# Kernel tuning notes

Hardware: AMD Instinct MI355X
Metric: run time of the kernel (lower is better)

Reference implementation:

```python
import jax, jax.numpy as jnp
import numpy as np

NODE_TYPES = ["patient", "visit", "symptom", "procedure", "disease", "drug"]
N = {"patient": 20000, "visit": 100000, "symptom": 4000, "procedure": 8000,
     "disease": 10000, "drug": 4000}
D = 128          # embedding_dim == hidden_channels
N_LAYERS = 4     # conv1..conv4
# (src, dst) per relation; reverse edges included so every node type gets messages
REL = [("patient", "visit"), ("visit", "patient"),
       ("visit", "symptom"), ("symptom", "visit"),
       ("visit", "procedure"), ("procedure", "visit"),
       ("visit", "disease"), ("disease", "visit"),
       ("visit", "drug"), ("drug", "visit")]
E_FWD = {("patient", "visit"): 100000, ("visit", "symptom"): 300000,
         ("visit", "procedure"): 200000, ("visit", "disease"): 250000,
         ("visit", "drug"): 300000}
EI_NAMES = ["ei_pv", "ei_vp", "ei_vs", "ei_sv", "ei_vpr", "ei_prv",
            "ei_vd", "ei_dv", "ei_vdr", "ei_drv"]
E_LABEL = 200000


def setup_inputs() -> dict:
    key = jax.random.key(0)
    ks = iter(jax.random.split(key, 64))
    inp = {}
    for nt in NODE_TYPES:
        inp[f"node_id_{nt}"] = jnp.arange(N[nt], dtype=jnp.int32)
        inp[f"emb_{nt}"] = jax.random.normal(next(ks), (N[nt], D), jnp.float32)
    for name, (src, dst) in zip(EI_NAMES, REL):
        e = E_FWD.get((src, dst), E_FWD.get((dst, src)))
        row = jax.random.randint(next(ks), (e,), 0, N[src], dtype=jnp.int32)
        col = jax.random.randint(next(ks), (e,), 0, N[dst], dtype=jnp.int32)
        inp[name] = jnp.stack([row, col])
    R = len(REL)
    inp["W_l"] = jax.random.normal(next(ks), (N_LAYERS, R, D, D), jnp.float32) * 0.05
    inp["b_l"] = jnp.zeros((N_LAYERS, R, D), jnp.float32)
    inp["W_r"] = jax.random.normal(next(ks), (N_LAYERS, R, D, D), jnp.float32) * 0.05
    inp["cls_w1"] = jax.random.normal(next(ks), (2 * D, D), jnp.float32) * 0.05
    inp["cls_b1"] = jnp.zeros((D,), jnp.float32)
    inp["cls_w2"] = jax.random.normal(next(ks), (D, 1), jnp.float32) * 0.05
    inp["cls_b2"] = jnp.zeros((1,), jnp.float32)
    row = jax.random.randint(next(ks), (E_LABEL,), 0, N["visit"], dtype=jnp.int32)
    col = jax.random.randint(next(ks), (E_LABEL,), 0, N["drug"], dtype=jnp.int32)
    inp["edge_label_index"] = jnp.stack([row, col])
    inp["edge_label"] = jax.random.bernoulli(next(ks), 0.5, (E_LABEL,)).astype(jnp.float32)
    return inp


def _hetero_sage_layer(x, eis, Wl, bl, Wr):
    # to_hetero semantics: out[dst] = sum over edge types (src,rel,dst) of
    #   SAGEConv_rel: lin_l(mean_j x[src][j]) + lin_r(x[dst])   (PyG defaults)
    out = {nt: jnp.zeros_like(v) for nt, v in x.items()}
    for r, (src, dst) in enumerate(REL):
        ei = eis[r]
        n_dst = x[dst].shape[0]
        msg = jax.ops.segment_sum(x[src][ei[0]], ei[1], num_segments=n_dst)
        deg = jax.ops.segment_sum(jnp.ones((ei.shape[1],), x[src].dtype), ei[1],
                                  num_segments=n_dst)
        mean = msg / jnp.maximum(deg, 1.0)[:, None]  # empty segments stay 0 as in PyG
        out[dst] = out[dst] + mean @ Wl[r] + bl[r] + x[dst] @ Wr[r]
    return out


def reference(node_id_patient, node_id_visit, node_id_symptom, node_id_procedure,
              node_id_disease, node_id_drug,
              emb_patient, emb_visit, emb_symptom, emb_procedure, emb_disease, emb_drug,
              ei_pv, ei_vp, ei_vs, ei_sv, ei_vpr, ei_prv, ei_vd, ei_dv, ei_vdr, ei_drv,
              W_l, b_l, W_r, cls_w1, cls_b1, cls_w2, cls_b2,
              edge_label_index, edge_label):
    x = {"patient": emb_patient[node_id_patient],
         "visit": emb_visit[node_id_visit],
         "symptom": emb_symptom[node_id_symptom],
         "procedure": emb_procedure[node_id_procedure],
         "disease": emb_disease[node_id_disease],
         "drug": emb_drug[node_id_drug]}
    eis = [ei_pv, ei_vp, ei_vs, ei_sv, ei_vpr, ei_prv, ei_vd, ei_dv, ei_vdr, ei_drv]
    for l in range(N_LAYERS):
        x = _hetero_sage_layer(x, eis, W_l[l], b_l[l], W_r[l])
        if l < N_LAYERS - 1:  # relu after conv1..conv3 only; dropout is eval-mode identity
            x = {k: jax.nn.relu(v) for k, v in x.items()}
    # Classifier: gather visit/drug node features per labeled edge, concat, MLP
    zv = x["visit"][edge_label_index[0]]
    zd = x["drug"][edge_label_index[1]]
    h = jax.nn.relu(jnp.concatenate([zv, zd], axis=-1) @ cls_w1 + cls_b1)
    pred = (h @ cls_w2 + cls_b2).reshape(-1)
    # BCE with logits: softplus(z) - z*y, mean-reduced
    loss = jnp.mean(jax.nn.softplus(pred) - pred * edge_label)
    return loss, pred
```

## Files before the change

kernel.cpp:

```cpp
#include <hip/hip_runtime.h>
#include <cmath>


typedef _Float16 f16x8 __attribute__((ext_vector_type(8)));
typedef float f32x4 __attribute__((ext_vector_type(4)));

#define NREL 10
#define NCOUNTS 546000
#define NEDGES  2300000
#define NVISIT  100000
#define NVEDGES 1150000
#define PLW 546816
#define WT_ELEMS (4 * PLW + 69632)
#define XELEMS 18688000UL
#define SELEMS 5888000UL
#define NBKT 873
#define BCAP 5056

struct BkMeta {
  const int* ei[NREL]; int E[NREL]; int cbc[NREL]; int ndst[NREL];
  int sh[NREL]; int bb[NREL]; int nb[NREL];
};
struct PreMeta {
  const float* emb[6]; const int* nid[6]; int rows[6]; int off[6];
  const float* W_l; const float* b_l; const float* W_r; const float* cw1;
  _Float16* Wt; float* visitSumB;
};
struct MTask {
  const _Float16* AH0; const _Float16* AL0;
  const _Float16* AH1; const _Float16* AL1;
  const _Float16* W;
  const float* bias;
  _Float16* outH; _Float16* outL;
  int M, blkOff, K, relu;
};
struct MMeta { MTask t[6]; int nTasks; };
struct F1Meta {
  const int* rp[5]; _Float16* mH[5]; _Float16* mL[5]; int aM[5]; int aOff[5];
  int nAgg; int aggTotal;
  const _Float16* gAH[5]; const _Float16* gAL[5]; const _Float16* gW[5];
  _Float16* gY[5]; int gM[5]; int gOff[5]; int nG;
};

__global__ __launch_bounds__(256) void pre_all(PreMeta pm, BkMeta bm,
                                               _Float16* __restrict__ H,
                                               _Float16* __restrict__ L,
                                               int* __restrict__ bcur,
                                               int* __restrict__ bdata) {
  __shared__ int cnt[128];
  __shared__ int base[128];
  __shared__ unsigned short rnk[4096];
  int b = blockIdx.x;
  int tid = threadIdx.x;
  if (b < 37500) {
    int t = b / 6250;
    int i = (b % 6250) * 256 + tid;
    if (i >= pm.rows[t] * 16) return;
    int row = i >> 4, q = i & 15;
    int s = pm.nid[t][row];
    const float* p = pm.emb[t] + (size_t)s * 128 + q * 8;
    float4 v0 = *(const float4*)p;
    float4 v1 = *(const float4*)(p + 4);
    float v[8] = {v0.x, v0.y, v0.z, v0.w, v1.x, v1.y, v1.z, v1.w};
    f16x8 h, l;
    #pragma unroll
    for (int j = 0; j < 8; ++j) {
      h[j] = (_Float16)v[j];
      l[j] = (_Float16)(v[j] - (float)h[j]);
    }
    size_t o = (size_t)(pm.off[t] + row) * 128 + q * 8;
    *(f16x8*)(H + o) = h;
    *(f16x8*)(L + o) = l;
    return;
  }
  if (b < 41726) {
    const int visitRel[5] = {0, 3, 5, 7, 9};
    const int inRel[5] = {1, 2, 4, 6, 8};
    int gid = (b - 37500) * 256 + tid;
    if (gid < 1048576) {
      int l = gid >> 18, o = gid & 262143;
      float val; size_t wbase; int n, k, Kpad;
      if (o < 163840) {
        int t = o >> 15, e = o & 32767;
        k = e >> 7; n = e & 127; Kpad = 264;
        int r = inRel[t];
        val = (k < 128) ? pm.W_l[(size_t)(l * 10 + r) * 16384 + k * 128 + n]
                        : pm.W_r[(size_t)(l * 10 + r) * 16384 + (k - 128) * 128 + n];
        wbase = (size_t)l * PLW + t * 67584;
      } else if (o < 245760) {
        int q = (o - 163840) >> 14, e = (o - 163840) & 16383;
        k = e >> 7; n = e & 127; Kpad = 136;
        val = pm.W_l[(size_t)(l * 10 + visitRel[q]) * 16384 + k * 128 + n];
        wbase = (size_t)l * PLW + 337920 + q * 34816;
      } else {
        int e = o - 245760;
        k = e >> 7; n = e & 127; Kpad = 136;
        val = 0.f;
        #pragma unroll
        for (int q = 0; q < 5; ++q)
          val += pm.W_r[(size_t)(l * 10 + visitRel[q]) * 16384 + k * 128 + n];
        wbase = (size_t)l * PLW + 512000;
      }
      _Float16 h = (_Float16)val;
      _Float16 lo = (_Float16)(val - (float)h);
      pm.Wt[wbase + (size_t)n * Kpad + k] = h;
      pm.Wt[wbase + (size_t)(128 + n) * Kpad + k] = lo;
    } else if (gid < 1081344) {
      int e = gid - 1048576;
      int k = e >> 7, n = e & 127;
      float val = pm.cw1[(size_t)k * 128 + n];
      _Float16 h = (_Float16)val;
      _Float16 lo = (_Float16)(val - (float)h);
      size_t wbase = (size_t)4 * PLW + (k < 128 ? 0 : 34816);
      int kk = k & 127;
      pm.Wt[wbase + (size_t)n * 136 + kk] = h;
      pm.Wt[wbase + (size_t)(128 + n) * 136 + kk] = lo;
    } else if (gid < 1081856) {
      int e = gid - 1081344;
      int l = e >> 7, c = e & 127;
      float val = 0.f;
      #pragma unroll
      for (int q = 0; q < 5; ++q) val += pm.b_l[(l * 10 + visitRel[q]) * 128 + c];
      pm.visitSumB[e] = val;
    }
    return;
  }
  int fb = b - 41726;
  int r = fb / 74;
  int bx = fb - r * 74;
  int E = bm.E[r], sh = bm.sh[r], bb = bm.bb[r], nb = bm.nb[r];
  if (tid < 128) cnt[tid] = 0;
  __syncthreads();
  int e0 = bx * 4096;
  if (e0 >= E) return;
  const int* dstp = bm.ei[r] + E;
  const int* srcp = bm.ei[r];
  #pragma unroll
  for (int i = 0; i < 16; ++i) {
    int e = e0 + i * 256 + tid;
    if (e < E) {
      int bk = dstp[e] >> sh;
      rnk[i * 256 + tid] = (unsigned short)atomicAdd(&cnt[bk], 1);
    }
  }
  __syncthreads();
  if (tid < nb && cnt[tid] > 0) base[tid] = atomicAdd(&bcur[bb + tid], cnt[tid]);
  __syncthreads();
  #pragma unroll
  for (int i = 0; i < 16; ++i) {
    int e = e0 + i * 256 + tid;
    if (e < E) {
      int d = dstp[e];
      int bk = d >> sh;
      int pos = base[bk] + (int)rnk[i * 256 + tid];
      if (pos < BCAP)
        bdata[(size_t)(bb + bk) * BCAP + pos] = ((d & ((1 << sh) - 1)) << 17) | srcp[e];
    }
  }
}

__global__ __launch_bounds__(256) void bkt_p2a(BkMeta bm, const int* __restrict__ bcur,
                                               const int* __restrict__ bdata,
                                               int* __restrict__ counts) {
  __shared__ int hist[2048];
  int g = blockIdx.x;
  int r = 0;
  #pragma unroll
  for (int i = 1; i < NREL; ++i) if (g >= bm.bb[i]) r = i;
  int lb = g - bm.bb[r];
  int sh = bm.sh[r], dpb = 1 << sh;
  int tid = threadIdx.x;
  for (int d = tid; d < dpb; d += 256) hist[d] = 0;
  __syncthreads();
  int cnt = bcur[g]; if (cnt > BCAP) cnt = BCAP;
  const int* bd = bdata + (size_t)g * BCAP;
  for (int i = tid; i < cnt; i += 256) atomicAdd(&hist[((unsigned)bd[i]) >> 17], 1);
  __syncthreads();
  int dBase = lb << sh;
  int dMax = bm.ndst[r] - dBase; if (dMax > dpb) dMax = dpb;
  for (int d = tid; d < dMax; d += 256) counts[bm.cbc[r] + dBase + d] = hist[d];
}

__global__ __launch_bounds__(1024) void scan1(const int* __restrict__ counts,
                                              int* __restrict__ partials) {
  __shared__ int s[1024];
  int i = blockIdx.x * 1024 + threadIdx.x;
  s[threadIdx.x] = (i < NCOUNTS) ? counts[i] : 0;
  __syncthreads();
  for (int off = 512; off > 0; off >>= 1) {
    if (threadIdx.x < off) s[threadIdx.x] += s[threadIdx.x + off];
    __syncthreads();
  }
  if (threadIdx.x == 0) partials[blockIdx.x] = s[0];
}

__global__ __launch_bounds__(1024) void scan2(int* __restrict__ partials, int nb) {
  __shared__ int s[1024];
  int t = threadIdx.x;
  int v = (t < nb) ? partials[t] : 0;
  s[t] = v;
  __syncthreads();
  for (int off = 1; off < 1024; off <<= 1) {
    int add = (t >= off) ? s[t - off] : 0;
    __syncthreads();
    s[t] += add;
    __syncthreads();
  }
  if (t < nb) partials[t] = s[t] - v;
}

__global__ __launch_bounds__(1024) void scan3(const int* __restrict__ counts,
                                              int* __restrict__ prefix,
                                              const int* __restrict__ partials) {
  __shared__ int s[1024];
  int t = threadIdx.x;
  int i = blockIdx.x * 1024 + t;
  int v = (i < NCOUNTS) ? counts[i] : 0;
  s[t] = v;
  __syncthreads();
  for (int off = 1; off < 1024; off <<= 1) {
    int add = (t >= off) ? s[t - off] : 0;
    __syncthreads();
    s[t] += add;
    __syncthreads();
  }
  int P = partials[blockIdx.x] + s[t] - v;
  if (i < NCOUNTS) prefix[i] = P;
  if (blockIdx.x == 0 && t == 0) prefix[NCOUNTS] = NEDGES;
}

__global__ __launch_bounds__(256) void bkt_p2b(BkMeta bm, const int* __restrict__ bcur,
                                               const int* __restrict__ bdata,
                                               const int* __restrict__ prefix,
                                               int* __restrict__ esrc) {
  __shared__ int pk[BCAP];
  __shared__ int srt[BCAP];
  __shared__ int cur[2048];
  __shared__ int part[256];
  __shared__ int baseSh;
  int g = blockIdx.x;
  int r = 0;
  #pragma unroll
  for (int i = 1; i < NREL; ++i) if (g >= bm.bb[i]) r = i;
  int lb = g - bm.bb[r];
  int sh = bm.sh[r], dpb = 1 << sh;
  int tid = threadIdx.x;
  int cnt = bcur[g]; if (cnt > BCAP) cnt = BCAP;
  const int* bd = bdata + (size_t)g * BCAP;
  for (int d = tid; d < dpb; d += 256) cur[d] = 0;
  for (int i = tid; i < cnt; i += 256) pk[i] = bd[i];
  __syncthreads();
  for (int i = tid; i < cnt; i += 256) atomicAdd(&cur[((unsigned)pk[i]) >> 17], 1);
  __syncthreads();
  int seg = (dpb + 255) >> 8;
  int s = 0;
  int b0 = tid * seg;
  for (int j = 0; j < seg; ++j) {
    int idx = b0 + j;
    if (idx < dpb) { int v = cur[idx]; cur[idx] = s; s += v; }
  }
  part[tid] = s;
  __syncthreads();
  for (int off = 1; off < 256; off <<= 1) {
    int add = (tid >= off) ? part[tid - off] : 0;
    __syncthreads();
    part[tid] += add;
    __syncthreads();
  }
  int myoff = part[tid] - s;
  for (int j = 0; j < seg; ++j) {
    int idx = b0 + j;
    if (idx < dpb) cur[idx] += myoff;
  }
  if (tid == 0) baseSh = prefix[bm.cbc[r] + (lb << sh)];
  __syncthreads();
  for (int i = tid; i < cnt; i += 256) {
    int p = pk[i];
    int pos = atomicAdd(&cur[((unsigned)p) >> 17], 1);
    srt[pos] = p & 0x1FFFF;
  }
  __syncthreads();
  int base = baseSh;
  for (int i = tid; i < cnt; i += 256) esrc[base + i] = srt[i];
}

__global__ __launch_bounds__(256) void merge_visit(const int* __restrict__ prefix,
                                                   const int* __restrict__ esrc,
                                                   int* __restrict__ mprefix,
                                                   int2* __restrict__ mesrc) {
  const int cbc[5]  = {0, 124000, 232000, 342000, 446000};
  const int yoff[5] = {0, 20000, 24000, 32000, 42000};
  int v = blockIdx.x * 256 + threadIdx.x;
  if (v >= NVISIT) return;
  int e0[5], e1[5];
  int base = 0;
  #pragma unroll
  for (int q = 0; q < 5; ++q) {
    e0[q] = prefix[cbc[q] + v];
    e1[q] = prefix[cbc[q] + v + 1];
    base += e0[q] - prefix[cbc[q]];
  }
  mprefix[v] = base;
  if (v == NVISIT - 1) {
    int t = base;
    #pragma unroll
    for (int q = 0; q < 5; ++q) t += e1[q] - e0[q];
    mprefix[NVISIT] = t;
  }
  int pos = base;
  #pragma unroll
  for (int q = 0; q < 5; ++q) {
    int d = e1[q] - e0[q];
    if (d > 0) {
      int wb = __float_as_int(1.f / (float)d);
      for (int e = e0[q]; e < e1[q]; ++e)
        mesrc[pos++] = make_int2(yoff[q] + esrc[e], wb);
    }
  }
}

__global__ __launch_bounds__(256, 8) void fused1(F1Meta f,
                                                 const _Float16* __restrict__ xvH,
                                                 const int* __restrict__ esrc) {
  int b = blockIdx.x;
  int tid = threadIdx.x;
  if (b < f.aggTotal) {
    int t = 0;
    #pragma unroll
    for (int i = 1; i < 5; ++i) if (i < f.nAgg && b >= f.aOff[i]) t = i;
    int row = (b - f.aOff[t]) * 16 + (tid >> 4);
    if (row >= f.aM[t]) return;
    int q = tid & 15;
    const int* rp = f.rp[t];
    int e0 = rp[row], e1 = rp[row + 1];
    float a[8];
    #pragma unroll
    for (int j = 0; j < 8; ++j) a[j] = 0.f;
    int e = e0;
    for (; e + 4 <= e1; e += 4) {
      int s0 = esrc[e], s1 = esrc[e + 1], s2 = esrc[e + 2], s3 = esrc[e + 3];
      f16x8 v0 = *(const f16x8*)(xvH + (size_t)s0 * 128 + q * 8);
      f16x8 v1 = *(const f16x8*)(xvH + (size_t)s1 * 128 + q * 8);
      f16x8 v2 = *(const f16x8*)(xvH + (size_t)s2 * 128 + q * 8);
      f16x8 v3 = *(const f16x8*)(xvH + (size_t)s3 * 128 + q * 8);
      #pragma unroll
      for (int j = 0; j < 8; ++j)
        a[j] += ((float)v0[j] + (float)v1[j]) + ((float)v2[j] + (float)v3[j]);
    }
    for (; e < e1; ++e) {
      int s = esrc[e];
      f16x8 v = *(const f16x8*)(xvH + (size_t)s * 128 + q * 8);
      #pragma unroll
      for (int j = 0; j < 8; ++j) a[j] += (float)v[j];
    }
    float inv = (e1 > e0) ? 1.f / (float)(e1 - e0) : 0.f;
    f16x8 h, l;
    #pragma unroll
    for (int j = 0; j < 8; ++j) {
      float v = a[j] * inv;
      h[j] = (_Float16)v;
      l[j] = (_Float16)(v - (float)h[j]);
    }
    size_t o = (size_t)row * 128 + q * 8;
    *(f16x8*)(f.mH[t] + o) = h;
    *(f16x8*)(f.mL[t] + o) = l;
    return;
  }
  b -= f.aggTotal;
  int g = 0;
  #pragma unroll
  for (int i = 1; i < 5; ++i) if (i < f.nG && b >= f.gOff[i]) g = i;
  int blockRow = (b - f.gOff[g]) * 32;
  int lane = tid & 63, wave = tid >> 6;
  int quad = lane >> 4, lm = lane & 15;
  int wr = wave >> 1, wc = wave & 1;
  const _Float16* AH = f.gAH[g];
  const _Float16* AL = f.gAL[g];
  const _Float16* W = f.gW[g];
  int M = f.gM[g];
  int ar = blockRow + wr * 16 + lm;
  if (ar >= M) ar = M - 1;
  f32x4 acc[4];
  #pragma unroll
  for (int nt = 0; nt < 4; ++nt) acc[nt] = (f32x4){0.f, 0.f, 0.f, 0.f};
  for (int ks = 0; ks < 128; ks += 32) {
    f16x8 ah = *(const f16x8*)(AH + (size_t)ar * 128 + ks + quad * 8);
    f16x8 al = *(const f16x8*)(AL + (size_t)ar * 128 + ks + quad * 8);
    #pragma unroll
    for (int nt = 0; nt < 4; ++nt) {
      int n = wc * 64 + nt * 16 + lm;
      f16x8 bh = *(const f16x8*)(W + (size_t)n * 136 + ks + quad * 8);
      f16x8 bl = *(const f16x8*)(W + (size_t)(128 + n) * 136 + ks + quad * 8);
      acc[nt] = __builtin_amdgcn_mfma_f32_16x16x32_f16(ah, bh, acc[nt], 0, 0, 0);
      acc[nt] = __builtin_amdgcn_mfma_f32_16x16x32_f16(ah, bl, acc[nt], 0, 0, 0);
      acc[nt] = __builtin_amdgcn_mfma_f32_16x16x32_f16(al, bh, acc[nt], 0, 0, 0);
    }
  }
  _Float16* Y = f.gY[g];
  #pragma unroll
  for (int i = 0; i < 4; ++i) {
    int grow = blockRow + wr * 16 + quad * 4 + i;
    if (grow >= M) continue;
    #pragma unroll
    for (int nt = 0; nt < 4; ++nt)
      Y[(size_t)grow * 128 + wc * 64 + nt * 16 + lm] = (_Float16)acc[nt][i];
  }
}

__global__ __launch_bounds__(256) void agg_visit(const int* __restrict__ mprefix,
                                                 const int2* __restrict__ mesrc,
                                                 const _Float16* __restrict__ YH,
                                                 _Float16* __restrict__ xvH,
                                                 _Float16* __restrict__ xvL, int doRelu) {
  int row = blockIdx.x * 16 + (threadIdx.x >> 4);
  if (row >= NVISIT) return;
  int q = threadIdx.x & 15;
  size_t o = (size_t)row * 128 + q * 8;
  f16x8 h0 = *(f16x8*)(xvH + o);
  f16x8 l0 = *(f16x8*)(xvL + o);
  float a[8];
  #pragma unroll
  for (int j = 0; j < 8; ++j) a[j] = (float)h0[j] + (float)l0[j];
  int e0 = mprefix[row], e1 = mprefix[row + 1];
  int e = e0;
  for (; e + 4 <= e1; e += 4) {
    int2 p0 = mesrc[e], p1 = mesrc[e + 1], p2 = mesrc[e + 2], p3 = mesrc[e + 3];
    f16x8 v0 = *(const f16x8*)(YH + (size_t)p0.x * 128 + q * 8);
    f16x8 v1 = *(const f16x8*)(YH + (size_t)p1.x * 128 + q * 8);
    f16x8 v2 = *(const f16x8*)(YH + (size_t)p2.x * 128 + q * 8);
    f16x8 v3 = *(const f16x8*)(YH + (size_t)p3.x * 128 + q * 8);
    float w0 = __int_as_float(p0.y), w1 = __int_as_float(p1.y);
    float w2 = __int_as_float(p2.y), w3 = __int_as_float(p3.y);
    #pragma unroll
    for (int j = 0; j < 8; ++j)
      a[j] += (w0 * (float)v0[j] + w1 * (float)v1[j]) +
              (w2 * (float)v2[j] + w3 * (float)v3[j]);
  }
  for (; e < e1; ++e) {
    int2 p = mesrc[e];
    f16x8 v = *(const f16x8*)(YH + (size_t)p.x * 128 + q * 8);
    float w = __int_as_float(p.y);
    #pragma unroll
    for (int j = 0; j < 8; ++j) a[j] += w * (float)v[j];
  }
  f16x8 h, l;
  #pragma unroll
  for (int j = 0; j < 8; ++j) {
    float v = doRelu ? fmaxf(a[j], 0.f) : a[j];
    h[j] = (_Float16)v;
    l[j] = (_Float16)(v - (float)h[j]);
  }
  *(f16x8*)(xvH + o) = h;
  *(f16x8*)(xvL + o) = l;
}

__global__ __launch_bounds__(256, 2) void mgemm(MMeta mm) {
  int b = blockIdx.x;
  int ti = 0;
  for (int i = 1; i < mm.nTasks; ++i) if (b >= mm.t[i].blkOff) ti = i;
  MTask tk = mm.t[ti];
  int blockRow = (b - tk.blkOff) * 128;
  int Kpad = tk.K + 8;

  __shared__ _Float16 Ash[2][128][72];
  int tid = threadIdx.x;
  int wave = tid >> 6, lane = tid & 63;
  int quad = lane >> 4, lm = lane & 15;
  int wr = wave >> 1, wc = wave & 1;

  f32x4 acc[4][4];
  #pragma unroll
  for (int i = 0; i < 4; ++i)
    #pragma unroll
    for (int j = 0; j < 4; ++j) acc[i][j] = (f32x4){0.f, 0.f, 0.f, 0.f};

  const _Float16* wrowH[4];
  const _Float16* wrowL[4];
  #pragma unroll
  for (int nt = 0; nt < 4; ++nt) {
    int n = wc * 64 + nt * 16 + lm;
    wrowH[nt] = tk.W + (size_t)n * Kpad;
    wrowL[nt] = tk.W + (size_t)(128 + n) * Kpad;
  }

  int sr = tid >> 1, sk = (tid & 1) * 32;
  int gr = blockRow + sr; if (gr >= tk.M) gr = tk.M - 1;
  for (int k0 = 0; k0 < tk.K; k0 += 64) {
    const _Float16* AH = (k0 < 128) ? tk.AH0 : tk.AH1;
    const _Float16* AL = (k0 < 128) ? tk.AL0 : tk.AL1;
    size_t abase = (size_t)gr * 128 + (k0 & 127) + sk;
    #pragma unroll
    for (int c = 0; c < 4; ++c) {
      *(f16x8*)&Ash[0][sr][sk + c * 8] = *(const f16x8*)(AH + abase + c * 8);
      *(f16x8*)&Ash[1][sr][sk + c * 8] = *(const f16x8*)(AL + abase + c * 8);
    }
    __syncthreads();
    #pragma unroll
    for (int ks = 0; ks < 64; ks += 32) {
      int kf = k0 + ks + quad * 8;
      f16x8 bh[4], bl[4];
      #pragma unroll
      for (int nt = 0; nt < 4; ++nt) {
        bh[nt] = *(const f16x8*)(wrowH[nt] + kf);
        bl[nt] = *(const f16x8*)(wrowL[nt] + kf);
      }
      #pragma unroll
      for (int mt = 0; mt < 4; ++mt) {
        int r = wr * 64 + mt * 16 + lm;
        f16x8 ah = *(const f16x8*)&Ash[0][r][ks + quad * 8];
        f16x8 al = *(const f16x8*)&Ash[1][r][ks + quad * 8];
        #pragma unroll
        for (int nt = 0; nt < 4; ++nt) {
          acc[mt][nt] = __builtin_amdgcn_mfma_f32_16x16x32_f16(ah, bh[nt], acc[mt][nt], 0, 0, 0);
          acc[mt][nt] = __builtin_amdgcn_mfma_f32_16x16x32_f16(ah, bl[nt], acc[mt][nt], 0, 0, 0);
          acc[mt][nt] = __builtin_amdgcn_mfma_f32_16x16x32_f16(al, bh[nt], acc[mt][nt], 0, 0, 0);
        }
      }
    }
    __syncthreads();
  }

  float bv[4];
  #pragma unroll
  for (int nt = 0; nt < 4; ++nt)
    bv[nt] = tk.bias ? tk.bias[wc * 64 + nt * 16 + lm] : 0.f;
  #pragma unroll
  for (int mt = 0; mt < 4; ++mt) {
    #pragma unroll
    for (int i = 0; i < 4; ++i) {
      int grow = blockRow + wr * 64 + mt * 16 + quad * 4 + i;
      if (grow >= tk.M) continue;
      size_t ob = (size_t)grow * 128 + wc * 64 + lm;
      #pragma unroll
      for (int nt = 0; nt < 4; ++nt) {
        float v = acc[mt][nt][i] + bv[nt];
        if (tk.relu) v = fmaxf(v, 0.f);
        _Float16 h = (_Float16)v;
        tk.outH[ob + nt * 16] = h;
        if (tk.outL) tk.outL[ob + nt * 16] = (_Float16)(v - (float)h);
      }
    }
  }
}

__global__ __launch_bounds__(256) void cls_edge(
    const _Float16* __restrict__ UH, const _Float16* __restrict__ UL,
    const _Float16* __restrict__ VH, const _Float16* __restrict__ VL,
    const int* __restrict__ eli, const float* __restrict__ w2,
    const float* __restrict__ b2, const float* __restrict__ y,
    float* __restrict__ lossOut, float* __restrict__ pred, int M) {
  __shared__ float lsum[4];
  int tid = threadIdx.x;
  int q = tid & 15;
  int lane = tid & 63;
  float w2v[8];
  #pragma unroll
  for (int j = 0; j < 8; ++j) w2v[j] = w2[q * 8 + j];
  float bias = b2[0];
  float lacc = 0.f;
  int e0 = blockIdx.x * 128 + (tid >> 4);
  #pragma unroll
  for (int p = 0; p < 8; ++p) {
    int e = e0 + p * 16;
    if (e < M) {
      int vi = eli[e], di = eli[M + e];
      size_t uo = (size_t)vi * 128 + q * 8;
      size_t vo = (size_t)di * 128 + q * 8;
      f16x8 uh = *(const f16x8*)(UH + uo);
      f16x8 ul = *(const f16x8*)(UL + uo);
      f16x8 vh = *(const f16x8*)(VH + vo);
      f16x8 vl = *(const f16x8*)(VL + vo);
      float part = 0.f;
      #pragma unroll
      for (int j = 0; j < 8; ++j) {
        float t = ((float)uh[j] + (float)ul[j]) + ((float)vh[j] + (float)vl[j]);
        part += fmaxf(t, 0.f) * w2v[j];
      }
      part += __shfl_xor(part, 1);
      part += __shfl_xor(part, 2);
      part += __shfl_xor(part, 4);
      part += __shfl_xor(part, 8);
      if (q == 0) {
        float z = part + bias;
        pred[e] = z;
        lacc += fmaxf(z, 0.f) + log1pf(expf(-fabsf(z))) - z * y[e];
      }
    }
  }
  lacc += __shfl_xor(lacc, 16);
  lacc += __shfl_xor(lacc, 32);
  if (lane == 0) lsum[tid >> 6] = lacc;
  __syncthreads();
  if (tid == 0)
    atomicAdd(lossOut, (lsum[0] + lsum[1] + lsum[2] + lsum[3]) * (1.0f / 200000.0f));
}

extern "C" void kernel_launch(void* const* d_in, const int* in_sizes, int n_in,
                              void* d_out, int out_size, void* d_ws, size_t ws_size,
                              hipStream_t stream) {
  static const int kRows[6] = {20000, 100000, 4000, 8000, 10000, 4000};
  static const int kOff[6]  = {0, 20000, 120000, 124000, 132000, 142000};
  static const int kSmallT[5]   = {0, 2, 3, 4, 5};
  static const int kInRel[5]    = {1, 2, 4, 6, 8};
  static const int kCbcIn[5]    = {100000, 120000, 224000, 332000, 442000};
  static const int kYOff[5]     = {0, 20000, 24000, 32000, 42000};
  static const int kBOff[5]     = {0, 157, 189, 252, 331};
  static const int kAggOff[5]   = {0, 1250, 1500, 2000, 2625};
  static const int kLeanOff[5]  = {0, 625, 750, 1000, 1313};
  const int kAggTotal = 2875, kLeanTotal = 1438;
  static const int kCbcA[NREL]  = {0, 100000, 120000, 124000, 224000,
                                   232000, 332000, 342000, 442000, 446000};
  static const int kEhA[NREL]   = {100000, 100000, 300000, 300000, 200000,
                                   200000, 250000, 250000, 300000, 300000};
  static const int kNdst[NREL]  = {100000, 20000, 4000, 100000, 8000,
                                   100000, 10000, 100000, 4000, 100000};
  static const int kSh[NREL]    = {11, 9, 5, 10, 7, 10, 7, 10, 5, 10};
  static const int kNB[NREL]    = {49, 40, 125, 98, 63, 98, 79, 98, 125, 98};
  static const int kBB[NREL]    = {0, 49, 89, 214, 312, 375, 473, 552, 650, 775};

  const float* W_l = (const float*)d_in[22];
  const float* b_l = (const float*)d_in[23];
  const float* W_r = (const float*)d_in[24];
  const float* cw1 = (const float*)d_in[25];
  const float* cb1 = (const float*)d_in[26];
  const float* cw2 = (const float*)d_in[27];
  const float* cb2 = (const float*)d_in[28];
  const int* eli = (const int*)d_in[29];
  const float* ylab = (const float*)d_in[30];

  _Float16* H = (_Float16*)d_ws;
  _Float16* L = H + XELEMS;
  _Float16* meanH = L + XELEMS;
  _Float16* meanL = meanH + SELEMS;
  _Float16* YH = meanL + SELEMS;
  _Float16* Wt = YH + SELEMS;
  int* prefix = (int*)(Wt + WT_ELEMS);
  int* counts = prefix + 546004;
  int* esrc = counts + NCOUNTS;
  int* partials = esrc + NEDGES;
  float* visitSumB = (float*)(partials + 1024);
  int* bcur = (int*)(visitSumB + 512);
  int* bdata = bcur + 1024;

  int* mprefix = counts;
  int2* mesrc = (int2*)bdata;

  _Float16* UH = meanH;
  _Float16* VH = meanH + (size_t)NVISIT * 128;
  _Float16* VL = VH + (size_t)4000 * 128;
  _Float16* UL = (_Float16*)prefix;

  BkMeta bm;
  for (int r = 0; r < NREL; ++r) {
    bm.ei[r] = (const int*)d_in[12 + r];
    bm.E[r] = kEhA[r];
    bm.cbc[r] = kCbcA[r];
    bm.ndst[r] = kNdst[r];
    bm.sh[r] = kSh[r];
    bm.bb[r] = kBB[r];
    bm.nb[r] = kNB[r];
  }

  hipMemsetAsync(bcur, 0, NBKT * sizeof(int), stream);
  hipMemsetAsync(d_out, 0, sizeof(float), stream);

  PreMeta pm;
  for (int t = 0; t < 6; ++t) {
    pm.nid[t] = (const int*)d_in[2 * t];
    pm.emb[t] = (const float*)d_in[2 * t + 1];
    pm.rows[t] = kRows[t];
    pm.off[t] = kOff[t];
  }
  pm.W_l = W_l; pm.b_l = b_l; pm.W_r = W_r; pm.cw1 = cw1;
  pm.Wt = Wt; pm.visitSumB = visitSumB;
  pre_all<<<dim3(42466), 256, 0, stream>>>(pm, bm, H, L, bcur, bdata);

  bkt_p2a<<<dim3(NBKT), 256, 0, stream>>>(bm, bcur, bdata, counts);
  scan1<<<534, 1024, 0, stream>>>(counts, partials);
  scan2<<<1, 1024, 0, stream>>>(partials, 534);
  scan3<<<534, 1024, 0, stream>>>(counts, prefix, partials);
  bkt_p2b<<<dim3(NBKT), 256, 0, stream>>>(bm, bcur, bdata, prefix, esrc);
  merge_visit<<<dim3((NVISIT + 255) / 256), 256, 0, stream>>>(prefix, esrc, mprefix, mesrc);

  _Float16* xvH = H + (size_t)kOff[1] * 128;
  _Float16* xvL = L + (size_t)kOff[1] * 128;

  for (int l = 0; l < 4; ++l) {
    int doRelu = (l < 3);
    int last = (l == 3);
    _Float16* LW = Wt + (size_t)l * PLW;

    F1Meta f1;
    if (!last) {
      for (int t = 0; t < 5; ++t) {
        f1.rp[t] = prefix + kCbcIn[t];
        f1.mH[t] = meanH + (size_t)kYOff[t] * 128;
        f1.mL[t] = meanL + (size_t)kYOff[t] * 128;
        f1.aM[t] = kRows[kSmallT[t]];
        f1.aOff[t] = kAggOff[t];
      }
      f1.nAgg = 5;
      f1.aggTotal = kAggTotal;
    } else {
      f1.rp[0] = prefix + kCbcIn[4];
      f1.mH[0] = meanH + (size_t)kYOff[4] * 128;
      f1.mL[0] = meanL + (size_t)kYOff[4] * 128;
      f1.aM[0] = 4000;
      f1.aOff[0] = 0;
      for (int t = 1; t < 5; ++t) { f1.rp[t] = nullptr; f1.mH[t] = nullptr; f1.mL[t] = nullptr; f1.aM[t] = 0; f1.aOff[t] = 0; }
      f1.nAgg = 1;
      f1.aggTotal = 250;
    }
    for (int q = 0; q < 5; ++q) {
      size_t so = (size_t)kOff[kSmallT[q]] * 128;
      f1.gAH[q] = H + so;
      f1.gAL[q] = L + so;
      f1.gW[q] = LW + 337920 + (size_t)q * 34816;
      f1.gY[q] = YH + (size_t)kYOff[q] * 128;
      f1.gM[q] = kRows[kSmallT[q]];
      f1.gOff[q] = kLeanOff[q];
    }
    f1.nG = 5;
    fused1<<<dim3(f1.aggTotal + kLeanTotal), 256, 0, stream>>>(f1, xvH, esrc);

    MMeta m;
    if (!last) {
      m.nTasks = 6;
      for (int t = 0; t < 5; ++t) {
        size_t mo = (size_t)kYOff[t] * 128;
        size_t so = (size_t)kOff[kSmallT[t]] * 128;
        m.t[t].AH0 = meanH + mo; m.t[t].AL0 = meanL + mo;
        m.t[t].AH1 = H + so;     m.t[t].AL1 = L + so;
        m.t[t].W = LW + (size_t)t * 67584;
        m.t[t].bias = b_l + (size_t)(l * 10 + kInRel[t]) * 128;
        m.t[t].outH = H + so;    m.t[t].outL = L + so;
        m.t[t].M = kRows[kSmallT[t]];
        m.t[t].blkOff = kBOff[t];
        m.t[t].K = 256;
        m.t[t].relu = doRelu;
      }
      m.t[5].AH0 = xvH; m.t[5].AL0 = xvL;
      m.t[5].AH1 = nullptr; m.t[5].AL1 = nullptr;
      m.t[5].W = LW + 512000;
      m.t[5].bias = visitSumB + l * 128;
      m.t[5].outH = xvH; m.t[5].outL = xvL;
      m.t[5].M = NVISIT;
      m.t[5].blkOff = 363;
      m.t[5].K = 128;
      m.t[5].relu = 0;
      mgemm<<<dim3(363 + 782), 256, 0, stream>>>(m);
    } else {
      size_t mo = (size_t)kYOff[4] * 128;
      size_t so = (size_t)kOff[5] * 128;
      m.nTasks = 2;
      m.t[0].AH0 = meanH + mo; m.t[0].AL0 = meanL + mo;
      m.t[0].AH1 = H + so;     m.t[0].AL1 = L + so;
      m.t[0].W = LW + (size_t)4 * 67584;
      m.t[0].bias = b_l + (size_t)(l * 10 + kInRel[4]) * 128;
      m.t[0].outH = H + so;    m.t[0].outL = L + so;
      m.t[0].M = 4000;
      m.t[0].blkOff = 0;
      m.t[0].K = 256;
      m.t[0].relu = 0;
      m.t[1].AH0 = xvH; m.t[1].AL0 = xvL;
      m.t[1].AH1 = nullptr; m.t[1].AL1 = nullptr;
      m.t[1].W = LW + 512000;
      m.t[1].bias = visitSumB + l * 128;
      m.t[1].outH = xvH; m.t[1].outL = xvL;
      m.t[1].M = NVISIT;
      m.t[1].blkOff = 32;
      m.t[1].K = 128;
      m.t[1].relu = 0;
      mgemm<<<dim3(32 + 782), 256, 0, stream>>>(m);
    }

    agg_visit<<<dim3(6250), 256, 0, stream>>>(mprefix, mesrc, YH, xvH, xvL, doRelu);
  }

  MMeta muv;
  muv.nTasks = 2;
  muv.t[0].AH0 = xvH; muv.t[0].AL0 = xvL;
  muv.t[0].AH1 = nullptr; muv.t[0].AL1 = nullptr;
  muv.t[0].W = Wt + (size_t)4 * PLW;
  muv.t[0].bias = cb1;
  muv.t[0].outH = UH; muv.t[0].outL = UL;
  muv.t[0].M = NVISIT;
  muv.t[0].blkOff = 0;
  muv.t[0].K = 128;
  muv.t[0].relu = 0;
  muv.t[1].AH0 = H + (size_t)kOff[5] * 128; muv.t[1].AL0 = L + (size_t)kOff[5] * 128;
  muv.t[1].AH1 = nullptr; muv.t[1].AL1 = nullptr;
  muv.t[1].W = Wt + (size_t)4 * PLW + 34816;
  muv.t[1].bias = nullptr;
  muv.t[1].outH = VH; muv.t[1].outL = VL;
  muv.t[1].M = 4000;
  muv.t[1].blkOff = 782;
  muv.t[1].K = 128;
  muv.t[1].relu = 0;
  mgemm<<<dim3(782 + 32), 256, 0, stream>>>(muv);

  const int ML = 200000;
  cls_edge<<<dim3((ML + 127) / 128), 256, 0, stream>>>(
      UH, UL, VH, VL, eli, cw2, cb2, ylab,
      (float*)d_out, (float*)d_out + 1, ML);
}
```

Measured before the change: 909.1 us.

## Spread embedding fp16 conversion across bucket-sort kernels to overlap work

The embedding gather and hi/lo fp16 split is taken out of the first preprocessing kernel and spread as extra blocks across the bucket count, bucket sort and visit merge kernels. Conversion blocks are also packed densely by global row offset, so the padded per-type block grid is gone. The aim is to fill the idle CUs left by the small, latency-bound sort kernels with this bandwidth-bound work, and to shorten the critical first kernel. In exchange, the later kernels carry more blocks, and the merge kernel's grid now depends on the conversion share assigned to it.

```diff
diff --git a/kernel.cpp b/kernel.cpp
--- a/kernel.cpp
+++ b/kernel.cpp
@@ -16,13 +16,15 @@
 #define SELEMS 5888000UL
 #define NBKT 873
 #define BCAP 5056
+#define NMERGE 391
+#define CONV_BLKS 9125
 
 struct BkMeta {
   const int* ei[NREL]; int E[NREL]; int cbc[NREL]; int ndst[NREL];
   int sh[NREL]; int bb[NREL]; int nb[NREL];
 };
 struct PreMeta {
-  const float* emb[6]; const int* nid[6]; int rows[6]; int off[6];
+  const float* emb[6]; const int* nid[6]; int off[6];
   const float* W_l; const float* b_l; const float* W_r; const float* cw1;
   _Float16* Wt; float* visitSumB;
 };
@@ -42,92 +44,97 @@
   _Float16* gY[5]; int gM[5]; int gOff[5]; int nG;
 };
 
-__global__ __launch_bounds__(256) void pre_all(PreMeta pm, BkMeta bm,
-                                               _Float16* __restrict__ H,
-                                               _Float16* __restrict__ L,
-                                               int* __restrict__ bcur,
-                                               int* __restrict__ bdata) {
+__device__ __forceinline__ void conv0_body(const PreMeta& pm, int bc, int tid,
+                                           _Float16* __restrict__ H,
+                                           _Float16* __restrict__ L) {
+  int i = bc * 256 + tid;
+  if (i >= 146000 * 16) return;
+  int g = i >> 4, q = i & 15;
+  int t = 0;
+  #pragma unroll
+  for (int k = 1; k < 6; ++k) if (g >= pm.off[k]) t = k;
+  int row = g - pm.off[t];
+  int s = pm.nid[t][row];
+  const float* p = pm.emb[t] + (size_t)s * 128 + q * 8;
+  float4 v0 = *(const float4*)p;
+  float4 v1 = *(const float4*)(p + 4);
+  float v[8] = {v0.x, v0.y, v0.z, v0.w, v1.x, v1.y, v1.z, v1.w};
+  f16x8 h, l;
+  #pragma unroll
+  for (int j = 0; j < 8; ++j) {
+    h[j] = (_Float16)v[j];
+    l[j] = (_Float16)(v[j] - (float)h[j]);
+  }
+  size_t o = (size_t)g * 128 + q * 8;
+  *(f16x8*)(H + o) = h;
+  *(f16x8*)(L + o) = l;
+}
+
+__device__ __forceinline__ void prep_body(const PreMeta& pm, int gid) {
+  const int visitRel[5] = {0, 3, 5, 7, 9};
+  const int inRel[5] = {1, 2, 4, 6, 8};
+  if (gid < 1048576) {
+    int l = gid >> 18, o = gid & 262143;
+    float val; size_t wbase; int n, k, Kpad;
+    if (o < 163840) {
+      int t = o >> 15, e = o & 32767;
+      k = e >> 7; n = e & 127; Kpad = 264;
+      int r = inRel[t];
+      val = (k < 128) ? pm.W_l[(size_t)(l * 10 + r) * 16384 + k * 128 + n]
+                      : pm.W_r[(size_t)(l * 10 + r) * 16384 + (k - 128) * 128 + n];
+      wbase = (size_t)l * PLW + t * 67584;
+    } else if (o < 245760) {
+      int q = (o - 163840) >> 14, e = (o - 163840) & 16383;
+      k = e >> 7; n = e & 127; Kpad = 136;
+      val = pm.W_l[(size_t)(l * 10 + visitRel[q]) * 16384 + k * 128 + n];
+      wbase = (size_t)l * PLW + 337920 + q * 34816;
+    } else {
+      int e = o - 245760;
+      k = e >> 7; n = e & 127; Kpad = 136;
+      val = 0.f;
+      #pragma unroll
+      for (int q = 0; q < 5; ++q)
+        val += pm.W_r[(size_t)(l * 10 + visitRel[q]) * 16384 + k * 128 + n];
+      wbase = (size_t)l * PLW + 512000;
+    }
+    _Float16 h = (_Float16)val;
+    _Float16 lo = (_Float16)(val - (float)h);
+    pm.Wt[wbase + (size_t)n * Kpad + k] = h;
+    pm.Wt[wbase + (size_t)(128 + n) * Kpad + k] = lo;
+  } else if (gid < 1081344) {
+    int e = gid - 1048576;
+    int k = e >> 7, n = e & 127;
+    float val = pm.cw1[(size_t)k * 128 + n];
+    _Float16 h = (_Float16)val;
+    _Float16 lo = (_Float16)(val - (float)h);
+    size_t wbase = (size_t)4 * PLW + (k < 128 ? 0 : 34816);
+    int kk = k & 127;
+    pm.Wt[wbase + (size_t)n * 136 + kk] = h;
+    pm.Wt[wbase + (size_t)(128 + n) * 136 + kk] = lo;
+  } else if (gid < 1081856) {
+    int e = gid - 1081344;
+    int l = e >> 7, c = e & 127;
+    float val = 0.f;
+    #pragma unroll
+    for (int q = 0; q < 5; ++q) val += pm.b_l[(l * 10 + visitRel[q]) * 128 + c];
+    pm.visitSumB[e] = val;
+  }
+}
+
+__global__ __launch_bounds__(256) void k1_p1_prep(BkMeta bm, PreMeta pm,
+                                                  int* __restrict__ bcur,
+                                                  int* __restrict__ bdata) {
   __shared__ int cnt[128];
   __shared__ int base[128];
   __shared__ unsigned short rnk[4096];
   int b = blockIdx.x;
   int tid = threadIdx.x;
-  if (b < 37500) {
-    int t = b / 6250;
-    int i = (b % 6250) * 256 + tid;
-    if (i >= pm.rows[t] * 16) return;
-    int row = i >> 4, q = i & 15;
-    int s = pm.nid[t][row];
-    const float* p = pm.emb[t] + (size_t)s * 128 + q * 8;
-    float4 v0 = *(const float4*)p;
-    float4 v1 = *(const float4*)(p + 4);
-    float v[8] = {v0.x, v0.y, v0.z, v0.w, v1.x, v1.y, v1.z, v1.w};
-    f16x8 h, l;
-    #pragma unroll
-    for (int j = 0; j < 8; ++j) {
-      h[j] = (_Float16)v[j];
-      l[j] = (_Float16)(v[j] - (float)h[j]);
-    }
-    size_t o = (size_t)(pm.off[t] + row) * 128 + q * 8;
-    *(f16x8*)(H + o) = h;
-    *(f16x8*)(L + o) = l;
+  if (b >= 740) {
+    prep_body(pm, (b - 740) * 256 + tid);
     return;
   }
-  if (b < 41726) {
-    const int visitRel[5] = {0, 3, 5, 7, 9};
-    const int inRel[5] = {1, 2, 4, 6, 8};
-    int gid = (b - 37500) * 256 + tid;
-    if (gid < 1048576) {
-      int l = gid >> 18, o = gid & 262143;
-      float val; size_t wbase; int n, k, Kpad;
-      if (o < 163840) {
-        int t = o >> 15, e = o & 32767;
-        k = e >> 7; n = e & 127; Kpad = 264;
-        int r = inRel[t];
-        val = (k < 128) ? pm.W_l[(size_t)(l * 10 + r) * 16384 + k * 128 + n]
-                        : pm.W_r[(size_t)(l * 10 + r) * 16384 + (k - 128) * 128 + n];
-        wbase = (size_t)l * PLW + t * 67584;
-      } else if (o < 245760) {
-        int q = (o - 163840) >> 14, e = (o - 163840) & 16383;
-        k = e >> 7; n = e & 127; Kpad = 136;
-        val = pm.W_l[(size_t)(l * 10 + visitRel[q]) * 16384 + k * 128 + n];
-        wbase = (size_t)l * PLW + 337920 + q * 34816;
-      } else {
-        int e = o - 245760;
-        k = e >> 7; n = e & 127; Kpad = 136;
-        val = 0.f;
-        #pragma unroll
-        for (int q = 0; q < 5; ++q)
-          val += pm.W_r[(size_t)(l * 10 + visitRel[q]) * 16384 + k * 128 + n];
-        wbase = (size_t)l * PLW + 512000;
-      }
-      _Float16 h = (_Float16)val;
-      _Float16 lo = (_Float16)(val - (float)h);
-      pm.Wt[wbase + (size_t)n * Kpad + k] = h;
-      pm.Wt[wbase + (size_t)(128 + n) * Kpad + k] = lo;
-    } else if (gid < 1081344) {
-      int e = gid - 1048576;
-      int k = e >> 7, n = e & 127;
-      float val = pm.cw1[(size_t)k * 128 + n];
-      _Float16 h = (_Float16)val;
-      _Float16 lo = (_Float16)(val - (float)h);
-      size_t wbase = (size_t)4 * PLW + (k < 128 ? 0 : 34816);
-      int kk = k & 127;
-      pm.Wt[wbase + (size_t)n * 136 + kk] = h;
-      pm.Wt[wbase + (size_t)(128 + n) * 136 + kk] = lo;
-    } else if (gid < 1081856) {
-      int e = gid - 1081344;
-      int l = e >> 7, c = e & 127;
-      float val = 0.f;
-      #pragma unroll
-      for (int q = 0; q < 5; ++q) val += pm.b_l[(l * 10 + visitRel[q]) * 128 + c];
-      pm.visitSumB[e] = val;
-    }
-    return;
-  }
-  int fb = b - 41726;
-  int r = fb / 74;
-  int bx = fb - r * 74;
+  int r = b / 74;
+  int bx = b - r * 74;
   int E = bm.E[r], sh = bm.sh[r], bb = bm.bb[r], nb = bm.nb[r];
   if (tid < 128) cnt[tid] = 0;
   __syncthreads();
@@ -159,17 +166,26 @@
   }
 }
 
-__global__ __launch_bounds__(256) void bkt_p2a(BkMeta bm, const int* __restrict__ bcur,
-                                               const int* __restrict__ bdata,
-                                               int* __restrict__ counts) {
+__global__ __launch_bounds__(256) void k2_p2a_conv(BkMeta bm, PreMeta pm,
+                                                   const int* __restrict__ bcur,
+                                                   const int* __restrict__ bdata,
+                                                   int* __restrict__ counts,
+                                                   _Float16* __restrict__ H,
+                                                   _Float16* __restrict__ L,
+                                                   int convBase) {
   __shared__ int hist[2048];
-  int g = blockIdx.x;
+  int b = blockIdx.x;
+  int tid = threadIdx.x;
+  if (b >= NBKT) {
+    conv0_body(pm, convBase + b - NBKT, tid, H, L);
+    return;
+  }
+  int g = b;
   int r = 0;
   #pragma unroll
   for (int i = 1; i < NREL; ++i) if (g >= bm.bb[i]) r = i;
   int lb = g - bm.bb[r];
   int sh = bm.sh[r], dpb = 1 << sh;
-  int tid = threadIdx.x;
   for (int d = tid; d < dpb; d += 256) hist[d] = 0;
   __syncthreads();
   int cnt = bcur[g]; if (cnt > BCAP) cnt = BCAP;
@@ -229,22 +245,31 @@
   if (blockIdx.x == 0 && t == 0) prefix[NCOUNTS] = NEDGES;
 }
 
-__global__ __launch_bounds__(256) void bkt_p2b(BkMeta bm, const int* __restrict__ bcur,
-                                               const int* __restrict__ bdata,
-                                               const int* __restrict__ prefix,
-                                               int* __restrict__ esrc) {
+__global__ __launch_bounds__(256) void k3_p2b_conv(BkMeta bm, PreMeta pm,
+                                                   const int* __restrict__ bcur,
+                                                   const int* __restrict__ bdata,
+                                                   const int* __restrict__ prefix,
+                                                   int* __restrict__ esrc,
+                                                   _Float16* __restrict__ H,
+                                                   _Float16* __restrict__ L,
+                                                   int convBase) {
   __shared__ int pk[BCAP];
   __shared__ int srt[BCAP];
   __shared__ int cur[2048];
   __shared__ int part[256];
   __shared__ int baseSh;
-  int g = blockIdx.x;
+  int b = blockIdx.x;
+  int tid = threadIdx.x;
+  if (b >= NBKT) {
+    conv0_body(pm, convBase + b - NBKT, tid, H, L);
+    return;
+  }
+  int g = b;
   int r = 0;
   #pragma unroll
   for (int i = 1; i < NREL; ++i) if (g >= bm.bb[i]) r = i;
   int lb = g - bm.bb[r];
   int sh = bm.sh[r], dpb = 1 << sh;
-  int tid = threadIdx.x;
   int cnt = bcur[g]; if (cnt > BCAP) cnt = BCAP;
   const int* bd = bdata + (size_t)g * BCAP;
   for (int d = tid; d < dpb; d += 256) cur[d] = 0;
@@ -284,13 +309,23 @@
   for (int i = tid; i < cnt; i += 256) esrc[base + i] = srt[i];
 }
 
-__global__ __launch_bounds__(256) void merge_visit(const int* __restrict__ prefix,
-                                                   const int* __restrict__ esrc,
-                                                   int* __restrict__ mprefix,
-                                                   int2* __restrict__ mesrc) {
+__global__ __launch_bounds__(256) void k4_merge_conv(PreMeta pm,
+                                                     const int* __restrict__ prefix,
+                                                     const int* __restrict__ esrc,
+                                                     int* __restrict__ mprefix,
+                                                     int2* __restrict__ mesrc,
+                                                     _Float16* __restrict__ H,
+                                                     _Float16* __restrict__ L,
+                                                     int convBase) {
+  int b = blockIdx.x;
+  int tid = threadIdx.x;
+  if (b >= NMERGE) {
+    conv0_body(pm, convBase + b - NMERGE, tid, H, L);
+    return;
+  }
   const int cbc[5]  = {0, 124000, 232000, 342000, 446000};
   const int yoff[5] = {0, 20000, 24000, 32000, 42000};
-  int v = blockIdx.x * 256 + threadIdx.x;
+  int v = b * 256 + tid;
   if (v >= NVISIT) return;
   int e0[5], e1[5];
   int base = 0;
@@ -608,6 +643,7 @@
   static const int kAggOff[5]   = {0, 1250, 1500, 2000, 2625};
   static const int kLeanOff[5]  = {0, 625, 750, 1000, 1313};
   const int kAggTotal = 2875, kLeanTotal = 1438;
+  const int kConvK2 = 3000, kConvK3 = 1500, kConvK4 = CONV_BLKS - 4500;
   static const int kCbcA[NREL]  = {0, 100000, 120000, 124000, 224000,
                                    232000, 332000, 342000, 442000, 446000};
   static const int kEhA[NREL]   = {100000, 100000, 300000, 300000, 200000,
@@ -661,26 +697,29 @@
     bm.nb[r] = kNB[r];
   }
 
-  hipMemsetAsync(bcur, 0, NBKT * sizeof(int), stream);
-  hipMemsetAsync(d_out, 0, sizeof(float), stream);
-
   PreMeta pm;
   for (int t = 0; t < 6; ++t) {
     pm.nid[t] = (const int*)d_in[2 * t];
     pm.emb[t] = (const float*)d_in[2 * t + 1];
-    pm.rows[t] = kRows[t];
     pm.off[t] = kOff[t];
   }
   pm.W_l = W_l; pm.b_l = b_l; pm.W_r = W_r; pm.cw1 = cw1;
   pm.Wt = Wt; pm.visitSumB = visitSumB;
-  pre_all<<<dim3(42466), 256, 0, stream>>>(pm, bm, H, L, bcur, bdata);
-
-  bkt_p2a<<<dim3(NBKT), 256, 0, stream>>>(bm, bcur, bdata, counts);
+
+  hipMemsetAsync(bcur, 0, NBKT * sizeof(int), stream);
+  hipMemsetAsync(d_out, 0, sizeof(float), stream);
+
+  k1_p1_prep<<<dim3(740 + 4226), 256, 0, stream>>>(bm, pm, bcur, bdata);
+  k2_p2a_conv<<<dim3(NBKT + kConvK2), 256, 0, stream>>>(bm, pm, bcur, bdata,
+                                                        counts, H, L, 0);
   scan1<<<534, 1024, 0, stream>>>(counts, partials);
   scan2<<<1, 1024, 0, stream>>>(partials, 534);
   scan3<<<534, 1024, 0, stream>>>(counts, prefix, partials);
-  bkt_p2b<<<dim3(NBKT), 256, 0, stream>>>(bm, bcur, bdata, prefix, esrc);
-  merge_visit<<<dim3((NVISIT + 255) / 256), 256, 0, stream>>>(prefix, esrc, mprefix, mesrc);
+  k3_p2b_conv<<<dim3(NBKT + kConvK3), 256, 0, stream>>>(bm, pm, bcur, bdata,
+                                                        prefix, esrc, H, L, kConvK2);
+  k4_merge_conv<<<dim3(NMERGE + kConvK4), 256, 0, stream>>>(pm, prefix, esrc,
+                                                            mprefix, mesrc, H, L,
+                                                            kConvK2 + kConvK3);
 
   _Float16* xvH = H + (size_t)kOff[1] * 128;
   _Float16* xvL = L + (size_t)kOff[1] * 128;
```

After: 905.2 us (median of 2 runs). About the same (-0.4%).
